# Kernel optimization log

Measured on AMD Instinct MI355X. Metric: run time of the kernel, lower is better.

The kernel has to match this reference:

```python
import jax, jax.numpy as jnp
import numpy as np

PAD = -100

def _make_offsets(key, batch, src_len, n_words, valid_len):
    ofs = jnp.sort(jax.random.randint(key, (batch, src_len), 0, n_words), axis=1)
    # ensure max valid offset is n_words-1 so target_length == max+1
    ofs = ofs.at[:, valid_len - 1].set(n_words - 1)
    pos = jnp.arange(src_len)[None, :]
    return jnp.where(pos < valid_len, ofs, PAD).astype(jnp.int64)

def setup_inputs() -> dict:
    key = jax.random.key(0)
    k1, k2 = jax.random.split(key)
    batch, src_len, dim = 8, 4096, 1024
    n_words = 2048
    valid_len = src_len - 256  # trailing PAD region
    hidden_states = jax.random.normal(k1, (batch, src_len, dim), dtype=jnp.float32)
    word_offsets = _make_offsets(k2, batch, src_len, n_words, valid_len)
    return {"hidden_states": hidden_states, "word_offsets": word_offsets,
            "target_length": n_words}

def reference(hidden_states, word_offsets, target_length):
    # Faithful to WordPooler with take=_take_first: for each word, gather the
    # FIRST subword token (stop at first -100), then scatter-mean per word
    # (include_self=False -> untouched words stay zero).
    B, S, D = hidden_states.shape
    T = target_length
    # 'break' semantics: everything after the first PAD is invalid
    valid = jnp.cumprod((word_offsets != PAD).astype(jnp.int32), axis=1).astype(bool)
    prev = jnp.concatenate(
        [jnp.full((B, 1), -1, dtype=word_offsets.dtype), word_offsets[:, :-1]], axis=1)
    first = valid & (word_offsets != prev)  # [B, S] first-token-of-word mask
    # route non-selected tokens to a dump bucket (index T per batch)
    tgt = jnp.where(first, word_offsets, T)
    flat_tgt = (jnp.arange(B)[:, None] * (T + 1) + tgt).reshape(-1)  # [B*S]
    flat_h = hidden_states.reshape(B * S, D)
    w = first.reshape(-1).astype(hidden_states.dtype)  # selection weights
    sums = jnp.zeros((B * (T + 1), D), dtype=hidden_states.dtype)
    sums = sums.at[flat_tgt].add(flat_h * w[:, None])
    counts = jnp.zeros((B * (T + 1),), dtype=hidden_states.dtype).at[flat_tgt].add(w)
    out = sums / jnp.maximum(counts, 1.0)[:, None]  # zero-count words stay 0
    return out.reshape(B, T + 1, D)[:, :T, :]
```

## Files before the change

kernel.cpp:

```cpp
#include <hip/hip_runtime.h>


__global__ void __launch_bounds__(256)
wp_search_kernel(const int* __restrict__ ofs, int* __restrict__ src,
                 int S, int T) {
    const int t = blockIdx.x * 256 + threadIdx.x;
    const int b = blockIdx.y;
    if (t >= T) return;
    const int* __restrict__ row = ofs + (size_t)b * S;
    int lo = 0, hi = S;
    while (lo < hi) {
        int mid = (lo + hi) >> 1;
        int v = row[mid];
        int key = (v < 0) ? 0x7fffffff : v;
        if (key < t) lo = mid + 1; else hi = mid;
    }
    src[(size_t)b * T + t] = (lo < S && row[lo] == t) ? lo : -1;
}

__global__ void __launch_bounds__(256)
wp_gather_kernel(const float* __restrict__ hs, const int* __restrict__ src,
                 float* __restrict__ out, int S, int T, int D) {
    const int wave = threadIdx.x >> 6;
    const int lane = threadIdx.x & 63;
    const int t = blockIdx.x * 4 + wave;
    const int b = blockIdx.y;
    const size_t word = (size_t)b * T + t;
    const int s = src[word];
    const int nv = D >> 2;
    float4* __restrict__ o = (float4*)(out + word * (size_t)D);
    if (s >= 0) {
        const float4* __restrict__ in =
            (const float4*)(hs + ((size_t)b * S + s) * (size_t)D);
        #pragma unroll 4
        for (int j = lane; j < nv; j += 64) o[j] = in[j];
    } else {
        const float4 z = make_float4(0.f, 0.f, 0.f, 0.f);
        #pragma unroll 4
        for (int j = lane; j < nv; j += 64) o[j] = z;
    }
}

extern "C" void kernel_launch(void* const* d_in, const int* in_sizes, int n_in,
                              void* d_out, int out_size, void* d_ws, size_t ws_size,
                              hipStream_t stream) {
    const float* hs  = (const float*)d_in[0];
    const int*   ofs = (const int*)d_in[1];
    float* out = (float*)d_out;
    int* src = (int*)d_ws;

    const int B = 8;
    const int BS = in_sizes[1];
    const int S = BS / B;
    const int D = in_sizes[0] / BS;
    const int T = out_size / (B * D);

    dim3 g1((T + 255) / 256, B);
    wp_search_kernel<<<g1, 256, 0, stream>>>(ofs, src, S, T);

    dim3 g2(T / 4, B);
    wp_gather_kernel<<<g2, 256, 0, stream>>>(hs, src, out, S, T, D);
}
```

Measured before the change: 28.34 us.

## Fuse word search and gather into one token-chunk kernel

Replaces the two-kernel pipeline (a per-word binary search writing a source index table, then a gather) with a single kernel. Each block takes 16 tokens, loads their offsets into shared memory, finds the range of words those tokens cover, maps each word to its first token by a local binary search, and copies the row or writes zeros. This removes one launch and the round trip of the index table through global memory. In exchange, blocks covering the trailing PAD region exit early, and per-block work varies with how many words each chunk spans.

```diff
diff --git a/kernel.cpp b/kernel.cpp
--- a/kernel.cpp
+++ b/kernel.cpp
@@ -1,43 +1,77 @@
 #include <hip/hip_runtime.h>
 
 
-__global__ void __launch_bounds__(256)
-wp_search_kernel(const int* __restrict__ ofs, int* __restrict__ src,
-                 int S, int T) {
-    const int t = blockIdx.x * 256 + threadIdx.x;
-    const int b = blockIdx.y;
-    if (t >= T) return;
-    const int* __restrict__ row = ofs + (size_t)b * S;
-    int lo = 0, hi = S;
-    while (lo < hi) {
-        int mid = (lo + hi) >> 1;
-        int v = row[mid];
-        int key = (v < 0) ? 0x7fffffff : v;
-        if (key < t) lo = mid + 1; else hi = mid;
-    }
-    src[(size_t)b * T + t] = (lo < S && row[lo] == t) ? lo : -1;
-}
+typedef float v4f __attribute__((ext_vector_type(4)));
+
+#define TOK 16
+#define WCAP 256
 
 __global__ void __launch_bounds__(256)
-wp_gather_kernel(const float* __restrict__ hs, const int* __restrict__ src,
-                 float* __restrict__ out, int S, int T, int D) {
-    const int wave = threadIdx.x >> 6;
-    const int lane = threadIdx.x & 63;
-    const int t = blockIdx.x * 4 + wave;
-    const int b = blockIdx.y;
-    const size_t word = (size_t)b * T + t;
-    const int s = src[word];
+wp_fused(const float* __restrict__ hs, const int* __restrict__ ofs,
+         float* __restrict__ out, int S, int T, int D) {
+    const int b   = blockIdx.y;
+    const int s0  = blockIdx.x * TOK;
+    const int tid = threadIdx.x;
+    const int* __restrict__ row = ofs + (size_t)b * S;
+
+    __shared__ int w_ofs[TOK + 1];
+    __shared__ int w_src[WCAP];
+
+    if (tid <= TOK) {
+        int idx = s0 - 1 + tid;
+        w_ofs[tid] = (idx < 0) ? -1 : row[idx];
+    }
+    __syncthreads();
+
+    const int v_before = w_ofs[0];
+    if (v_before < -1) return;
+
+    const int lane = tid & 63;
+    const int wave = tid >> 6;
+
+    const bool my_valid = (lane < TOK) && (w_ofs[lane + 1] >= 0);
+    const unsigned long long mask = __ballot(my_valid);
+    if (mask == 0ULL) return;
+    const int j_last = (63 - __clzll(mask)) + 1;
+    const int v_last = w_ofs[j_last];
+    const int nw = v_last - v_before;
+    if (nw <= 0) return;
+
     const int nv = D >> 2;
-    float4* __restrict__ o = (float4*)(out + word * (size_t)D);
-    if (s >= 0) {
-        const float4* __restrict__ in =
-            (const float4*)(hs + ((size_t)b * S + s) * (size_t)D);
-        #pragma unroll 4
-        for (int j = lane; j < nv; j += 64) o[j] = in[j];
-    } else {
-        const float4 z = make_float4(0.f, 0.f, 0.f, 0.f);
-        #pragma unroll 4
-        for (int j = lane; j < nv; j += 64) o[j] = z;
+
+    for (int base = 0; base < nw; base += WCAP) {
+        const int lim = (nw - base < WCAP) ? (nw - base) : WCAP;
+
+        __syncthreads();
+        for (int wi = tid; wi < lim; wi += 256) {
+            const int w = v_before + 1 + base + wi;
+            int lo = 1, hi = TOK + 1;
+            while (lo < hi) {
+                int mid = (lo + hi) >> 1;
+                int v = w_ofs[mid];
+                int key = (v < 0) ? 0x7fffffff : v;
+                if (key < w) lo = mid + 1; else hi = mid;
+            }
+            const bool hit = (lo <= TOK) && (w_ofs[lo] == w);
+            w_src[wi] = hit ? (s0 - 1 + lo) : -1;
+        }
+        __syncthreads();
+
+        for (int wi = wave; wi < lim; wi += 4) {
+            const int s = w_src[wi];
+            const int t = v_before + 1 + base + wi;
+            v4f* __restrict__ o = (v4f*)(out + ((size_t)b * T + t) * (size_t)D);
+            if (s >= 0) {
+                const v4f* __restrict__ in =
+                    (const v4f*)(hs + ((size_t)b * S + s) * (size_t)D);
+                #pragma unroll 4
+                for (int j = lane; j < nv; j += 64) o[j] = in[j];
+            } else {
+                const v4f z = (v4f)(0.f);
+                #pragma unroll 4
+                for (int j = lane; j < nv; j += 64) o[j] = z;
+            }
+        }
     }
 }
 
@@ -47,7 +81,6 @@
     const float* hs  = (const float*)d_in[0];
     const int*   ofs = (const int*)d_in[1];
     float* out = (float*)d_out;
-    int* src = (int*)d_ws;
 
     const int B = 8;
     const int BS = in_sizes[1];
@@ -55,9 +88,6 @@
     const int D = in_sizes[0] / BS;
     const int T = out_size / (B * D);
 
-    dim3 g1((T + 255) / 256, B);
-    wp_search_kernel<<<g1, 256, 0, stream>>>(ofs, src, S, T);
-
-    dim3 g2(T / 4, B);
-    wp_gather_kernel<<<g2, 256, 0, stream>>>(hs, src, out, S, T, D);
+    dim3 grid(S / TOK, B);
+    wp_fused<<<grid, 256, 0, stream>>>(hs, ofs, out, S, T, D);
 }
```

Measured after the change: 57.84 us. 104% more time.
